# Kernel tuning notes

Measured on AMD Instinct MI355X. Metric: run time of the kernel, lower is better.

## Reference

```python
import jax, jax.numpy as jnp
import numpy as np
import math

D_MODEL = 512
N_HEADS = 8
D_K = D_MODEL // N_HEADS
N_SAMPLES = 16
BETA = 1.0
SCALE = 1.0 / math.sqrt(D_K)
PROPOSAL_TEMP = 0.5


def setup_inputs() -> dict:
    key = jax.random.key(0)
    ks = jax.random.split(key, 9)
    B, S = 2, 512
    x = jax.random.normal(ks[0], (B, S, D_MODEL), dtype=jnp.float32)
    init = lambda k: jax.random.normal(k, (D_MODEL, D_MODEL), dtype=jnp.float32) * 0.02
    return {
        "x": x,
        "Wq": init(ks[1]), "bq": jnp.zeros((D_MODEL,), jnp.float32),
        "Wk": init(ks[2]), "bk": jnp.zeros((D_MODEL,), jnp.float32),
        "Wv": init(ks[3]), "bv": jnp.zeros((D_MODEL,), jnp.float32),
        "Wo": init(ks[4]), "bo": jnp.zeros((D_MODEL,), jnp.float32),
    }


def _importance_sampled_weights(scores):
    # scores: [B,H,S,S]. Replicates the per-row Python loop, fully vectorized.
    B, H, Sq, Sk = scores.shape
    target = jax.nn.softmax(scores * BETA, axis=-1)            # [B,H,Sq,Sk]
    # optimal proposal: 0.5*target + 0.5*uniform
    prop = PROPOSAL_TEMP * target + (1.0 - PROPOSAL_TEMP) / Sk
    R = B * H * Sq
    tf = target.reshape(R, Sk)
    pf = prop.reshape(R, Sk)
    # tsu_backend.sample_binary_layer(log(p/(1-p))) == Bernoulli(p) sampling
    s = jax.random.bernoulli(jax.random.key(42), pf[:, None, :], (R, N_SAMPLES, Sk))
    # importance weight = prod(target[sel]) / (prod(prop[sel]) * prod(1-prop[~sel]))
    pt = jnp.prod(jnp.where(s, tf[:, None, :], 1.0), axis=-1)                 # [R,N]
    pp = jnp.prod(jnp.where(s, pf[:, None, :], 1.0 - pf[:, None, :]), axis=-1)
    valid = (s.sum(-1) > 0) & (pp > 0)
    w = jnp.where(valid, pt / jnp.maximum(pp, 1e-38), 0.0)
    ws = w.sum(-1, keepdims=True)
    w = jnp.where(ws > 0, w / jnp.maximum(ws, 1e-38), 1.0 / N_SAMPLES)        # [R,N]
    wa = jnp.einsum('rn,rnk->rk', w, s.astype(jnp.float32))                   # [R,Sk]
    was = wa.sum(-1, keepdims=True)
    wa = jnp.where(was > 0, wa / jnp.maximum(was, 1e-38), 1.0 / Sk)
    return wa.reshape(B, H, Sq, Sk)


def reference(x, Wq, bq, Wk, bk, Wv, bv, Wo, bo):
    B, S, Dm = x.shape
    proj = lambda W, b: (x @ W + b).reshape(B, S, N_HEADS, D_K).transpose(0, 2, 1, 3)
    Q = proj(Wq, bq)  # [B,H,S,dk]
    K = proj(Wk, bk)
    V = proj(Wv, bv)
    scores = jnp.einsum('bhqd,bhkd->bhqk', Q, K) * SCALE
    # torch builds weights via torch.tensor(...) which detaches => constant w.r.t. params
    attn = jax.lax.stop_gradient(_importance_sampled_weights(scores))
    out = jnp.einsum('bhqk,bhkd->bhqd', attn, V)
    out = out.transpose(0, 2, 1, 3).reshape(B, S, Dm)
    return out @ Wo + bo
```

## Files before the change

### kernel.cpp

```cpp
#include <hip/hip_runtime.h>
#include <cstdint>
#include <cstddef>


#define ROTL(x, r) __builtin_rotateleft32((x), (r))

#define QR8(s)                                                                \
  x0[0]+=x1[0];x0[1]+=x1[1];x0[2]+=x1[2];x0[3]+=x1[3];                        \
  x0[4]+=x1[4];x0[5]+=x1[5];x0[6]+=x1[6];x0[7]+=x1[7];                        \
  x1[0]=ROTL(x1[0],s);x1[1]=ROTL(x1[1],s);x1[2]=ROTL(x1[2],s);                \
  x1[3]=ROTL(x1[3],s);x1[4]=ROTL(x1[4],s);x1[5]=ROTL(x1[5],s);                \
  x1[6]=ROTL(x1[6],s);x1[7]=ROTL(x1[7],s);                                    \
  x1[0]^=x0[0];x1[1]^=x0[1];x1[2]^=x0[2];x1[3]^=x0[3];                        \
  x1[4]^=x0[4];x1[5]^=x0[5];x1[6]^=x0[6];x1[7]^=x0[7];
#define INJ8(X, Y)                                                            \
  x0[0]+=(X);x0[1]+=(X);x0[2]+=(X);x0[3]+=(X);                                \
  x0[4]+=(X);x0[5]+=(X);x0[6]+=(X);x0[7]+=(X);                                \
  x1[0]+=(Y);x1[1]+=(Y);x1[2]+=(Y);x1[3]+=(Y);                                \
  x1[4]+=(Y);x1[5]+=(Y);x1[6]+=(Y);x1[7]+=(Y);
#define INJ8Y(Y)                                                              \
  x1[0]+=(Y);x1[1]+=(Y);x1[2]+=(Y);x1[3]+=(Y);                                \
  x1[4]+=(Y);x1[5]+=(Y);x1[6]+=(Y);x1[7]+=(Y);

__global__ __launch_bounds__(256)
void qkv_gemm(const float* __restrict__ x,
              const float* __restrict__ Wq, const float* __restrict__ bq,
              const float* __restrict__ Wk, const float* __restrict__ bk,
              const float* __restrict__ Wv, const float* __restrict__ bv,
              const float* __restrict__ bo, float* __restrict__ outp,
              float* __restrict__ Qw, float* __restrict__ KTw,
              float* __restrict__ Vw) {
  const int tid = threadIdx.x;
  if (blockIdx.z == 3) {
    const int blk = blockIdx.y * 16 + blockIdx.x;
    const size_t base4 = (size_t)blk * 1024 + tid;
    const float4* bo4 = (const float4*)bo;
    float4* out4 = (float4*)outp;
#pragma unroll
    for (int i = 0; i < 4; ++i) {
      const size_t idx4 = base4 + (size_t)i * 256;
      out4[idx4] = bo4[idx4 & 127];
    }
    return;
  }
  const float* W; const float* bias;
  if (blockIdx.z == 0)      { W = Wq; bias = bq; }
  else if (blockIdx.z == 1) { W = Wk; bias = bk; }
  else                      { W = Wv; bias = bv; }

  __shared__ __align__(16) float smem[64 * 68];
  float (*At)[68] = (float(*)[68])smem;
  float (*Bs)[64] = (float(*)[64])(smem + 32 * 68);
  float (*T2)[68] = (float(*)[68])smem;

  const int tx = tid & 15, ty = tid >> 4;
  const int row0 = blockIdx.x * 64, col0 = blockIdx.y * 64;
  float acc[4][4] = {};

  for (int kk = 0; kk < 512; kk += 32) {
    const int ar = tid >> 2;
#pragma unroll
    for (int i = 0; i < 2; ++i) {
      const int kc = ((tid & 3) << 3) + (i << 2);
      const float4 a4 =
          *(const float4*)&x[(size_t)(row0 + ar) * 512 + kk + kc];
      At[kc + 0][ar] = a4.x; At[kc + 1][ar] = a4.y;
      At[kc + 2][ar] = a4.z; At[kc + 3][ar] = a4.w;
    }
#pragma unroll
    for (int i = 0; i < 2; ++i) {
      const int idx = tid + (i << 8);
      const int br = idx >> 4, bc = (idx & 15) << 2;
      *(float4*)&Bs[br][bc] =
          *(const float4*)&W[(size_t)(kk + br) * 512 + col0 + bc];
    }
    __syncthreads();
#pragma unroll
    for (int p = 0; p < 32; ++p) {
      const float4 a4 = *(const float4*)&At[p][ty << 2];
      const float4 b4 = *(const float4*)&Bs[p][tx << 2];
      acc[0][0] = fmaf(a4.x, b4.x, acc[0][0]); acc[0][1] = fmaf(a4.x, b4.y, acc[0][1]);
      acc[0][2] = fmaf(a4.x, b4.z, acc[0][2]); acc[0][3] = fmaf(a4.x, b4.w, acc[0][3]);
      acc[1][0] = fmaf(a4.y, b4.x, acc[1][0]); acc[1][1] = fmaf(a4.y, b4.y, acc[1][1]);
      acc[1][2] = fmaf(a4.y, b4.z, acc[1][2]); acc[1][3] = fmaf(a4.y, b4.w, acc[1][3]);
      acc[2][0] = fmaf(a4.z, b4.x, acc[2][0]); acc[2][1] = fmaf(a4.z, b4.y, acc[2][1]);
      acc[2][2] = fmaf(a4.z, b4.z, acc[2][2]); acc[2][3] = fmaf(a4.z, b4.w, acc[2][3]);
      acc[3][0] = fmaf(a4.w, b4.x, acc[3][0]); acc[3][1] = fmaf(a4.w, b4.y, acc[3][1]);
      acc[3][2] = fmaf(a4.w, b4.z, acc[3][2]); acc[3][3] = fmaf(a4.w, b4.w, acc[3][3]);
    }
    __syncthreads();
  }

  if (blockIdx.z == 0) {
#pragma unroll
    for (int i = 0; i < 4; ++i) {
      const int row = row0 + (ty << 2) + i;
      const int b = row >> 9, s = row & 511;
#pragma unroll
      for (int j = 0; j < 4; ++j) {
        const int col = col0 + (tx << 2) + j;
        const int h = col >> 6, d = col & 63;
        Qw[(((size_t)(b * 8 + h) * 512 + s) * 64) + d] = acc[i][j] + bias[col];
      }
    }
  } else if (blockIdx.z == 1) {
#pragma unroll
    for (int i = 0; i < 4; ++i) {
#pragma unroll
      for (int j = 0; j < 4; ++j) {
        const int col = col0 + (tx << 2) + j;
        T2[(tx << 2) + j][(ty << 2) + i] = acc[i][j] + bias[col];
      }
    }
    __syncthreads();
    const int c = tid >> 2, seg = tid & 3;
    const int b = row0 >> 9, h = blockIdx.y;
    const int s0 = (row0 & 511) + (seg << 4);
    float* dst = KTw + (((size_t)(b * 8 + h) * 64 + c) << 9) + s0;
#pragma unroll
    for (int i2 = 0; i2 < 4; ++i2) {
      *(float4*)&dst[i2 << 2] = *(const float4*)&T2[c][(seg << 4) + (i2 << 2)];
    }
  } else {
#pragma unroll
    for (int i = 0; i < 4; ++i) {
      const int row = row0 + (ty << 2) + i;
      const int b = row >> 9, s = row & 511;
#pragma unroll
      for (int j = 0; j < 4; ++j) {
        const int col = col0 + (tx << 2) + j;
        const int h = col >> 6, d = col & 63;
        Vw[(((size_t)(b * 8 + h) * 512 + s) * 64) + d] = acc[i][j] + bias[col];
      }
    }
  }
}

__global__ __launch_bounds__(256)
void fused_sample(const float* __restrict__ Q, const float* __restrict__ KT,
                  const float* __restrict__ V, const float* __restrict__ Wo,
                  float* __restrict__ outp) {
  const int r = ((blockIdx.x & 7) << 10) + (blockIdx.x >> 3);
  const int bh = r >> 9, q = r & 511;
  const int b = r >> 12, h = (r >> 9) & 7;
  const int tid = threadIdx.x;
  __shared__ __align__(16) float qs[64];
  __shared__ float red[8];
  __shared__ float tf[512];
  __shared__ __align__(16) uint32_t pscu2[512];
  __shared__ float wa[512];
  __shared__ float wr[16];
  __shared__ float redc[8];
  __shared__ float psum[4][64];
  __shared__ float o_s[64];
  __shared__ int   list[512];
  __shared__ int   cnt;

  if (tid == 0) cnt = 0;
  if (tid < 64) qs[tid] = Q[((size_t)bh * 512 + q) * 64 + tid];
  __syncthreads();

  float sc[2];
#pragma unroll
  for (int ii = 0; ii < 2; ++ii) {
    const int k = tid + (ii << 8);
    const float* Kp = KT + (size_t)bh * 64 * 512 + k;
    float s = 0.f;
#pragma unroll
    for (int d4 = 0; d4 < 16; ++d4) {
      const float4 qv = ((const float4*)qs)[d4];
      const float k0 = Kp[(size_t)(d4 * 4 + 0) * 512];
      const float k1 = Kp[(size_t)(d4 * 4 + 1) * 512];
      const float k2 = Kp[(size_t)(d4 * 4 + 2) * 512];
      const float k3 = Kp[(size_t)(d4 * 4 + 3) * 512];
      s = fmaf(qv.x, k0, s); s = fmaf(qv.y, k1, s);
      s = fmaf(qv.z, k2, s); s = fmaf(qv.w, k3, s);
    }
    sc[ii] = s * 0.125f;
  }
  float mx = fmaxf(sc[0], sc[1]);
  for (int m = 1; m < 64; m <<= 1) mx = fmaxf(mx, __shfl_xor(mx, m));
  if ((tid & 63) == 0) red[tid >> 6] = mx;
  __syncthreads();
  const float rowmax = fmaxf(fmaxf(red[0], red[1]), fmaxf(red[2], red[3]));
  const float e0 = expf(sc[0] - rowmax);
  const float e1 = expf(sc[1] - rowmax);
  float ssum = e0 + e1;
  for (int m = 1; m < 64; m <<= 1) ssum += __shfl_xor(ssum, m);
  if ((tid & 63) == 0) red[4 + (tid >> 6)] = ssum;
  __syncthreads();
  const float tot = red[4] + red[5] + red[6] + red[7];
  const float t0 = e0 / tot, t1 = e1 / tot;
  tf[tid] = t0; tf[tid + 256] = t1;
  wa[tid] = 0.f; wa[tid + 256] = 0.f;
  {
    const float p0 = fmaf(0.5f, t0, 0.0009765625f);
    const float p1 = fmaf(0.5f, t1, 0.0009765625f);
    {
      const int k = tid;
      pscu2[(((k & 31) >> 2) << 6) + ((k >> 5) << 2) + (k & 3)] =
          ((uint32_t)ceilf(p0 * 8388608.0f)) << 9;
    }
    {
      const int k = tid + 256;
      pscu2[(((k & 31) >> 2) << 6) + ((k >> 5) << 2) + (k & 3)] =
          ((uint32_t)ceilf(p1 * 8388608.0f)) << 9;
    }
    float ql = (1.f - p0) * (1.f - p1);
    for (int m = 1; m < 64; m <<= 1) ql *= __shfl_xor(ql, m);
    if ((tid & 63) == 0) redc[4 + (tid >> 6)] = ql;
  }
  __syncthreads();
  const float Qrow = redc[4] * redc[5] * redc[6] * redc[7];

  const int n = tid >> 4, t = tid & 15;
  const int k0i = t << 5;
  const uint32_t cbase =
      (uint32_t)r * 8192u + (uint32_t)n * 512u + (uint32_t)k0i + 42u;
  uint32_t bits = 0u;
#pragma unroll
  for (int jb = 0; jb < 32; jb += 8) {
    uint32_t x0[8], x1[8];
#pragma unroll
    for (int i = 0; i < 8; ++i) {
      const uint32_t c = cbase + (uint32_t)(jb + i);
      x0[i] = c;
      x1[i] = ROTL(c, 13) ^ c;
    }
    QR8(15) QR8(26) QR8(6)
    INJ8(42u, 0x1BD11BF1u)
    QR8(17) QR8(29) QR8(16) QR8(24)
    INJ8(0x1BD11BF0u, 2u)
    QR8(13) QR8(15) QR8(26) QR8(6)
    INJ8Y(45u)
    QR8(17) QR8(29) QR8(16) QR8(24)
    INJ8(42u, 0x1BD11BF4u)
    QR8(13) QR8(15) QR8(26) QR8(6)
    INJ8(0x1BD11BF0u, 5u)
    const uint4 pA = *(const uint4*)&pscu2[((jb >> 2) << 6) + (t << 2)];
    const uint4 pB = *(const uint4*)&pscu2[(((jb >> 2) + 1) << 6) + (t << 2)];
    bits |= (uint32_t)((x0[0] ^ x1[0]) < pA.x) << (jb + 0);
    bits |= (uint32_t)((x0[1] ^ x1[1]) < pA.y) << (jb + 1);
    bits |= (uint32_t)((x0[2] ^ x1[2]) < pA.z) << (jb + 2);
    bits |= (uint32_t)((x0[3] ^ x1[3]) < pA.w) << (jb + 3);
    bits |= (uint32_t)((x0[4] ^ x1[4]) < pB.x) << (jb + 4);
    bits |= (uint32_t)((x0[5] ^ x1[5]) < pB.y) << (jb + 5);
    bits |= (uint32_t)((x0[6] ^ x1[6]) < pB.z) << (jb + 6);
    bits |= (uint32_t)((x0[7] ^ x1[7]) < pB.w) << (jb + 7);
  }

  float ptl = 1.f, ratl = 1.f;
  int cl = __popc(bits);
  {
    uint32_t bb = bits;
    while (bb) {
      const int j = __builtin_ctz(bb);
      bb &= bb - 1u;
      const float tv = tf[k0i + j];
      const float p = fmaf(0.5f, tv, 0.0009765625f);
      ptl *= tv;
      ratl *= p / (1.f - p);
    }
  }
#pragma unroll
  for (int m = 1; m < 16; m <<= 1) {
    ptl *= __shfl_xor(ptl, m);
    ratl *= __shfl_xor(ratl, m);
    cl += __shfl_xor(cl, m);
  }
  if (t == 0) {
    const float pp = Qrow * ratl;
    wr[n] = (cl > 0 && pp > 0.f) ? (ptl / fmaxf(pp, 1e-38f)) : 0.f;
  }
  __syncthreads();
  float wsum = 0.f;
#pragma unroll
  for (int m2 = 0; m2 < 16; ++m2) wsum += wr[m2];
  const float wn = (wsum > 0.f) ? (wr[n] / fmaxf(wsum, 1e-38f)) : 0.0625f;
  {
    uint32_t bb = bits;
    while (bb) {
      const int j = __builtin_ctz(bb);
      bb &= bb - 1u;
      atomicAdd(&wa[k0i + j], wn);
    }
  }
  __syncthreads();

  float sp = wa[tid] + wa[tid + 256];
  for (int m = 1; m < 64; m <<= 1) sp += __shfl_xor(sp, m);
  if ((tid & 63) == 0) redc[tid >> 6] = sp;
  if (wa[tid] > 0.f)       { const int i = atomicAdd(&cnt, 1); list[i] = tid; }
  if (wa[tid + 256] > 0.f) { const int i = atomicAdd(&cnt, 1); list[i] = tid + 256; }
  __syncthreads();
  const float was = redc[0] + redc[1] + redc[2] + redc[3];
  const int nnz = cnt;

  const int g = tid >> 6, d = tid & 63;
  const float* Vb = V + ((size_t)(b * 8 + h) * 512) * 64;
  float acc = 0.f;
  if (was > 0.f) {
    const float inv = 1.f / fmaxf(was, 1e-38f);
    for (int i = g; i < nnz; i += 4) {
      const int k = list[i];
      acc = fmaf(wa[k] * inv, Vb[(size_t)k * 64 + d], acc);
    }
  } else {
    for (int k = g; k < 512; k += 4) acc += Vb[(size_t)k * 64 + d];
    acc *= 0.001953125f;
  }
  psum[g][d] = acc;
  __syncthreads();
  if (g == 0)
    o_s[d] = psum[0][d] + psum[1][d] + psum[2][d] + psum[3][d];
  __syncthreads();

  {
    const float* Wh = Wo + ((size_t)h * 64) * 512;
    float a0 = 0.f, a1 = 0.f;
#pragma unroll 8
    for (int dd = 0; dd < 64; ++dd) {
      const float ov = o_s[dd];
      a0 = fmaf(ov, Wh[(size_t)dd * 512 + tid], a0);
      a1 = fmaf(ov, Wh[(size_t)dd * 512 + tid + 256], a1);
    }
    float* orow = outp + ((size_t)(b * 512 + q)) * 512;
    atomicAdd(&orow[tid], a0);
    atomicAdd(&orow[tid + 256], a1);
  }
}

extern "C" void kernel_launch(void* const* d_in, const int* in_sizes, int n_in,
                              void* d_out, int out_size, void* d_ws,
                              size_t ws_size, hipStream_t stream) {
  const float* x  = (const float*)d_in[0];
  const float* Wq = (const float*)d_in[1];
  const float* bq = (const float*)d_in[2];
  const float* Wk = (const float*)d_in[3];
  const float* bk = (const float*)d_in[4];
  const float* Wv = (const float*)d_in[5];
  const float* bv = (const float*)d_in[6];
  const float* Wo = (const float*)d_in[7];
  const float* bo = (const float*)d_in[8];
  float* out = (float*)d_out;

  float* ws = (float*)d_ws;
  float* Qw = ws;
  float* KT = ws + 524288;
  float* Vw = ws + 1048576;

  dim3 gq(16, 8, 4);
  qkv_gemm<<<gq, 256, 0, stream>>>(x, Wq, bq, Wk, bk, Wv, bv, bo, out,
                                   Qw, KT, Vw);
  fused_sample<<<8192, 256, 0, stream>>>(Qw, KT, Vw, Wo, out);
}
```

Measured before the change: 253.0 us.

## Map one attention row per wavefront and register-prefetch smaller QKV GEMM tiles

The sampling kernel now handles four query rows per block, one per 64-lane wavefront, so block-wide __syncthreads and shared reductions become shuffles and wave-local LDS fences. Each lane computes eight scores with float4 K loads, builds 128 sample bits across two 64-bit masks, and does the Wo projection with eight accumulators using shuffled o values. The QKV GEMM uses 32-row tiles with register prefetch of the next k-slice to double the grid and overlap loads. The cost is more per-lane serial work (longer Philox loops and ctz loops) and reliance on wave-synchronous LDS semantics.

```diff
diff --git a/kernel.cpp b/kernel.cpp
--- a/kernel.cpp
+++ b/kernel.cpp
@@ -22,6 +22,8 @@
   x1[0]+=(Y);x1[1]+=(Y);x1[2]+=(Y);x1[3]+=(Y);                                \
   x1[4]+=(Y);x1[5]+=(Y);x1[6]+=(Y);x1[7]+=(Y);
 
+#define WAVE_FENCE() asm volatile("s_waitcnt lgkmcnt(0)" ::: "memory")
+
 __global__ __launch_bounds__(256)
 void qkv_gemm(const float* __restrict__ x,
               const float* __restrict__ Wq, const float* __restrict__ bq,
@@ -32,15 +34,12 @@
               float* __restrict__ Vw) {
   const int tid = threadIdx.x;
   if (blockIdx.z == 3) {
-    const int blk = blockIdx.y * 16 + blockIdx.x;
-    const size_t base4 = (size_t)blk * 1024 + tid;
+    const int blk = blockIdx.y * 32 + blockIdx.x;
+    const size_t base4 = (size_t)blk * 512 + tid;
     const float4* bo4 = (const float4*)bo;
     float4* out4 = (float4*)outp;
-#pragma unroll
-    for (int i = 0; i < 4; ++i) {
-      const size_t idx4 = base4 + (size_t)i * 256;
-      out4[idx4] = bo4[idx4 & 127];
-    }
+    out4[base4] = bo4[base4 & 127];
+    out4[base4 + 256] = bo4[(base4 + 256) & 127];
     return;
   }
   const float* W; const float* bias;
@@ -48,90 +47,81 @@
   else if (blockIdx.z == 1) { W = Wk; bias = bk; }
   else                      { W = Wv; bias = bv; }
 
-  __shared__ __align__(16) float smem[64 * 68];
-  float (*At)[68] = (float(*)[68])smem;
-  float (*Bs)[64] = (float(*)[64])(smem + 32 * 68);
-  float (*T2)[68] = (float(*)[68])smem;
+  __shared__ __align__(16) float smem[32 * 34 + 32 * 64];
+  float (*At)[34] = (float(*)[34])smem;
+  float (*Bs)[64] = (float(*)[64])(smem + 32 * 34);
+  float (*T2)[34] = (float(*)[34])smem;
 
   const int tx = tid & 15, ty = tid >> 4;
-  const int row0 = blockIdx.x * 64, col0 = blockIdx.y * 64;
-  float acc[4][4] = {};
+  const int row0 = blockIdx.x * 32, col0 = blockIdx.y * 64;
+  float acc[2][4] = {};
+
+  const int ar = tid >> 3;
+  const int kc = (tid & 7) << 2;
+  const int br0 = tid >> 4,         bc0 = (tid & 15) << 2;
+  const int br1 = (tid + 256) >> 4, bc1 = ((tid + 256) & 15) << 2;
+
+  float4 aR, bR0, bR1;
+  aR  = *(const float4*)&x[(size_t)(row0 + ar) * 512 + kc];
+  bR0 = *(const float4*)&W[(size_t)br0 * 512 + col0 + bc0];
+  bR1 = *(const float4*)&W[(size_t)br1 * 512 + col0 + bc1];
 
   for (int kk = 0; kk < 512; kk += 32) {
-    const int ar = tid >> 2;
+    At[kc + 0][ar] = aR.x; At[kc + 1][ar] = aR.y;
+    At[kc + 2][ar] = aR.z; At[kc + 3][ar] = aR.w;
+    *(float4*)&Bs[br0][bc0] = bR0;
+    *(float4*)&Bs[br1][bc1] = bR1;
+    __syncthreads();
+    if (kk < 480) {
+      const int kn = kk + 32;
+      aR  = *(const float4*)&x[(size_t)(row0 + ar) * 512 + kn + kc];
+      bR0 = *(const float4*)&W[(size_t)(kn + br0) * 512 + col0 + bc0];
+      bR1 = *(const float4*)&W[(size_t)(kn + br1) * 512 + col0 + bc1];
+    }
+#pragma unroll
+    for (int p = 0; p < 32; ++p) {
+      const float2 a2 = *(const float2*)&At[p][ty << 1];
+      const float4 b4 = *(const float4*)&Bs[p][tx << 2];
+      acc[0][0] = fmaf(a2.x, b4.x, acc[0][0]); acc[0][1] = fmaf(a2.x, b4.y, acc[0][1]);
+      acc[0][2] = fmaf(a2.x, b4.z, acc[0][2]); acc[0][3] = fmaf(a2.x, b4.w, acc[0][3]);
+      acc[1][0] = fmaf(a2.y, b4.x, acc[1][0]); acc[1][1] = fmaf(a2.y, b4.y, acc[1][1]);
+      acc[1][2] = fmaf(a2.y, b4.z, acc[1][2]); acc[1][3] = fmaf(a2.y, b4.w, acc[1][3]);
+    }
+    __syncthreads();
+  }
+
+  const int h = blockIdx.y;
+  if (blockIdx.z == 0 || blockIdx.z == 2) {
+    float* dst = (blockIdx.z == 0) ? Qw : Vw;
 #pragma unroll
     for (int i = 0; i < 2; ++i) {
-      const int kc = ((tid & 3) << 3) + (i << 2);
-      const float4 a4 =
-          *(const float4*)&x[(size_t)(row0 + ar) * 512 + kk + kc];
-      At[kc + 0][ar] = a4.x; At[kc + 1][ar] = a4.y;
-      At[kc + 2][ar] = a4.z; At[kc + 3][ar] = a4.w;
-    }
-#pragma unroll
-    for (int i = 0; i < 2; ++i) {
-      const int idx = tid + (i << 8);
-      const int br = idx >> 4, bc = (idx & 15) << 2;
-      *(float4*)&Bs[br][bc] =
-          *(const float4*)&W[(size_t)(kk + br) * 512 + col0 + bc];
-    }
-    __syncthreads();
-#pragma unroll
-    for (int p = 0; p < 32; ++p) {
-      const float4 a4 = *(const float4*)&At[p][ty << 2];
-      const float4 b4 = *(const float4*)&Bs[p][tx << 2];
-      acc[0][0] = fmaf(a4.x, b4.x, acc[0][0]); acc[0][1] = fmaf(a4.x, b4.y, acc[0][1]);
-      acc[0][2] = fmaf(a4.x, b4.z, acc[0][2]); acc[0][3] = fmaf(a4.x, b4.w, acc[0][3]);
-      acc[1][0] = fmaf(a4.y, b4.x, acc[1][0]); acc[1][1] = fmaf(a4.y, b4.y, acc[1][1]);
-      acc[1][2] = fmaf(a4.y, b4.z, acc[1][2]); acc[1][3] = fmaf(a4.y, b4.w, acc[1][3]);
-      acc[2][0] = fmaf(a4.z, b4.x, acc[2][0]); acc[2][1] = fmaf(a4.z, b4.y, acc[2][1]);
-      acc[2][2] = fmaf(a4.z, b4.z, acc[2][2]); acc[2][3] = fmaf(a4.z, b4.w, acc[2][3]);
-      acc[3][0] = fmaf(a4.w, b4.x, acc[3][0]); acc[3][1] = fmaf(a4.w, b4.y, acc[3][1]);
-      acc[3][2] = fmaf(a4.w, b4.z, acc[3][2]); acc[3][3] = fmaf(a4.w, b4.w, acc[3][3]);
-    }
-    __syncthreads();
-  }
-
-  if (blockIdx.z == 0) {
-#pragma unroll
-    for (int i = 0; i < 4; ++i) {
-      const int row = row0 + (ty << 2) + i;
+      const int row = row0 + (ty << 1) + i;
       const int b = row >> 9, s = row & 511;
 #pragma unroll
       for (int j = 0; j < 4; ++j) {
         const int col = col0 + (tx << 2) + j;
-        const int h = col >> 6, d = col & 63;
-        Qw[(((size_t)(b * 8 + h) * 512 + s) * 64) + d] = acc[i][j] + bias[col];
+        const int d = col & 63;
+        dst[(((size_t)(b * 8 + h) * 512 + s) * 64) + d] = acc[i][j] + bias[col];
       }
     }
-  } else if (blockIdx.z == 1) {
-#pragma unroll
-    for (int i = 0; i < 4; ++i) {
+  } else {
+#pragma unroll
+    for (int i = 0; i < 2; ++i) {
 #pragma unroll
       for (int j = 0; j < 4; ++j) {
         const int col = col0 + (tx << 2) + j;
-        T2[(tx << 2) + j][(ty << 2) + i] = acc[i][j] + bias[col];
+        T2[(tx << 2) + j][(ty << 1) + i] = acc[i][j] + bias[col];
       }
     }
     __syncthreads();
-    const int c = tid >> 2, seg = tid & 3;
-    const int b = row0 >> 9, h = blockIdx.y;
-    const int s0 = (row0 & 511) + (seg << 4);
-    float* dst = KTw + (((size_t)(b * 8 + h) * 64 + c) << 9) + s0;
-#pragma unroll
-    for (int i2 = 0; i2 < 4; ++i2) {
-      *(float4*)&dst[i2 << 2] = *(const float4*)&T2[c][(seg << 4) + (i2 << 2)];
-    }
-  } else {
-#pragma unroll
-    for (int i = 0; i < 4; ++i) {
-      const int row = row0 + (ty << 2) + i;
-      const int b = row >> 9, s = row & 511;
-#pragma unroll
-      for (int j = 0; j < 4; ++j) {
-        const int col = col0 + (tx << 2) + j;
-        const int h = col >> 6, d = col & 63;
-        Vw[(((size_t)(b * 8 + h) * 512 + s) * 64) + d] = acc[i][j] + bias[col];
-      }
+    const int b = row0 >> 9;
+    const int s0 = row0 & 511;
+#pragma unroll
+    for (int i2 = 0; i2 < 2; ++i2) {
+      const int idx = tid + (i2 << 8);
+      const int c = idx >> 3, seg = idx & 7;
+      float* dst = KTw + (((size_t)(b * 8 + h) * 64 + c) << 9) + s0 + (seg << 2);
+      *(float4*)dst = *(const float4*)&T2[c][seg << 2];
     }
   }
 }
@@ -140,90 +130,102 @@
 void fused_sample(const float* __restrict__ Q, const float* __restrict__ KT,
                   const float* __restrict__ V, const float* __restrict__ Wo,
                   float* __restrict__ outp) {
-  const int r = ((blockIdx.x & 7) << 10) + (blockIdx.x >> 3);
+  const int tid = threadIdx.x;
+  const int w = tid >> 6, l = tid & 63;
+  const int blk = blockIdx.x;
+  const int swz = ((blk & 7) << 8) | (blk >> 3);
+  const int r = (swz << 2) + w;
   const int bh = r >> 9, q = r & 511;
   const int b = r >> 12, h = (r >> 9) & 7;
-  const int tid = threadIdx.x;
-  __shared__ __align__(16) float qs[64];
-  __shared__ float red[8];
-  __shared__ float tf[512];
-  __shared__ __align__(16) uint32_t pscu2[512];
-  __shared__ float wa[512];
-  __shared__ float wr[16];
-  __shared__ float redc[8];
-  __shared__ float psum[4][64];
-  __shared__ float o_s[64];
-  __shared__ int   list[512];
-  __shared__ int   cnt;
-
-  if (tid == 0) cnt = 0;
-  if (tid < 64) qs[tid] = Q[((size_t)bh * 512 + q) * 64 + tid];
-  __syncthreads();
-
-  float sc[2];
-#pragma unroll
-  for (int ii = 0; ii < 2; ++ii) {
-    const int k = tid + (ii << 8);
-    const float* Kp = KT + (size_t)bh * 64 * 512 + k;
-    float s = 0.f;
-#pragma unroll
+
+  __shared__ __align__(16) float    qs[4][64];
+  __shared__ __align__(16) float    tfs[4][512];
+  __shared__ __align__(16) uint32_t thru[4][512];
+
+  float* tf = tfs[w];
+  uint32_t* thr = thru[w];
+  uint4* thr4 = (uint4*)thr;
+  float* wa = (float*)thr;
+
+  qs[w][l] = Q[((size_t)bh * 512 + q) * 64 + l];
+  WAVE_FENCE();
+
+  float s0 = 0.f, s1 = 0.f, s2 = 0.f, s3 = 0.f;
+  float s4 = 0.f, s5 = 0.f, s6 = 0.f, s7 = 0.f;
+  {
+    const float* Kp = KT + (size_t)bh * 64 * 512 + (l << 2);
+#pragma unroll 4
     for (int d4 = 0; d4 < 16; ++d4) {
-      const float4 qv = ((const float4*)qs)[d4];
-      const float k0 = Kp[(size_t)(d4 * 4 + 0) * 512];
-      const float k1 = Kp[(size_t)(d4 * 4 + 1) * 512];
-      const float k2 = Kp[(size_t)(d4 * 4 + 2) * 512];
-      const float k3 = Kp[(size_t)(d4 * 4 + 3) * 512];
-      s = fmaf(qv.x, k0, s); s = fmaf(qv.y, k1, s);
-      s = fmaf(qv.z, k2, s); s = fmaf(qv.w, k3, s);
-    }
-    sc[ii] = s * 0.125f;
-  }
-  float mx = fmaxf(sc[0], sc[1]);
+      const float4 qv = *(const float4*)&qs[w][d4 << 2];
+#pragma unroll
+      for (int c = 0; c < 4; ++c) {
+        const float qd = (c == 0) ? qv.x : (c == 1) ? qv.y : (c == 2) ? qv.z : qv.w;
+        const size_t off = (size_t)(d4 * 4 + c) * 512;
+        const float4 ka = *(const float4*)&Kp[off];
+        const float4 kb = *(const float4*)&Kp[off + 256];
+        s0 = fmaf(qd, ka.x, s0); s1 = fmaf(qd, ka.y, s1);
+        s2 = fmaf(qd, ka.z, s2); s3 = fmaf(qd, ka.w, s3);
+        s4 = fmaf(qd, kb.x, s4); s5 = fmaf(qd, kb.y, s5);
+        s6 = fmaf(qd, kb.z, s6); s7 = fmaf(qd, kb.w, s7);
+      }
+    }
+    s0 *= 0.125f; s1 *= 0.125f; s2 *= 0.125f; s3 *= 0.125f;
+    s4 *= 0.125f; s5 *= 0.125f; s6 *= 0.125f; s7 *= 0.125f;
+  }
+
+  float mx = fmaxf(fmaxf(fmaxf(s0, s1), fmaxf(s2, s3)),
+                   fmaxf(fmaxf(s4, s5), fmaxf(s6, s7)));
+#pragma unroll
   for (int m = 1; m < 64; m <<= 1) mx = fmaxf(mx, __shfl_xor(mx, m));
-  if ((tid & 63) == 0) red[tid >> 6] = mx;
-  __syncthreads();
-  const float rowmax = fmaxf(fmaxf(red[0], red[1]), fmaxf(red[2], red[3]));
-  const float e0 = expf(sc[0] - rowmax);
-  const float e1 = expf(sc[1] - rowmax);
-  float ssum = e0 + e1;
-  for (int m = 1; m < 64; m <<= 1) ssum += __shfl_xor(ssum, m);
-  if ((tid & 63) == 0) red[4 + (tid >> 6)] = ssum;
-  __syncthreads();
-  const float tot = red[4] + red[5] + red[6] + red[7];
-  const float t0 = e0 / tot, t1 = e1 / tot;
-  tf[tid] = t0; tf[tid + 256] = t1;
-  wa[tid] = 0.f; wa[tid + 256] = 0.f;
-  {
-    const float p0 = fmaf(0.5f, t0, 0.0009765625f);
-    const float p1 = fmaf(0.5f, t1, 0.0009765625f);
-    {
-      const int k = tid;
-      pscu2[(((k & 31) >> 2) << 6) + ((k >> 5) << 2) + (k & 3)] =
-          ((uint32_t)ceilf(p0 * 8388608.0f)) << 9;
-    }
-    {
-      const int k = tid + 256;
-      pscu2[(((k & 31) >> 2) << 6) + ((k >> 5) << 2) + (k & 3)] =
-          ((uint32_t)ceilf(p1 * 8388608.0f)) << 9;
-    }
-    float ql = (1.f - p0) * (1.f - p1);
-    for (int m = 1; m < 64; m <<= 1) ql *= __shfl_xor(ql, m);
-    if ((tid & 63) == 0) redc[4 + (tid >> 6)] = ql;
-  }
-  __syncthreads();
-  const float Qrow = redc[4] * redc[5] * redc[6] * redc[7];
-
-  const int n = tid >> 4, t = tid & 15;
-  const int k0i = t << 5;
+  const float e0 = expf(s0 - mx), e1 = expf(s1 - mx);
+  const float e2 = expf(s2 - mx), e3 = expf(s3 - mx);
+  const float e4 = expf(s4 - mx), e5 = expf(s5 - mx);
+  const float e6 = expf(s6 - mx), e7 = expf(s7 - mx);
+  float tot = ((e0 + e1) + (e2 + e3)) + ((e4 + e5) + (e6 + e7));
+#pragma unroll
+  for (int m = 1; m < 64; m <<= 1) tot += __shfl_xor(tot, m);
+  const float t0 = e0 / tot, t1 = e1 / tot, t2 = e2 / tot, t3 = e3 / tot;
+  const float t4 = e4 / tot, t5 = e5 / tot, t6 = e6 / tot, t7 = e7 / tot;
+  const float p0 = fmaf(0.5f, t0, 0.0009765625f);
+  const float p1 = fmaf(0.5f, t1, 0.0009765625f);
+  const float p2 = fmaf(0.5f, t2, 0.0009765625f);
+  const float p3 = fmaf(0.5f, t3, 0.0009765625f);
+  const float p4 = fmaf(0.5f, t4, 0.0009765625f);
+  const float p5 = fmaf(0.5f, t5, 0.0009765625f);
+  const float p6 = fmaf(0.5f, t6, 0.0009765625f);
+  const float p7 = fmaf(0.5f, t7, 0.0009765625f);
+  {
+    *(float4*)&tf[l << 2]         = make_float4(t0, t1, t2, t3);
+    *(float4*)&tf[256 + (l << 2)] = make_float4(t4, t5, t6, t7);
+    uint4 ta, tb;
+    ta.x = ((uint32_t)ceilf(p0 * 8388608.0f)) << 9;
+    ta.y = ((uint32_t)ceilf(p1 * 8388608.0f)) << 9;
+    ta.z = ((uint32_t)ceilf(p2 * 8388608.0f)) << 9;
+    ta.w = ((uint32_t)ceilf(p3 * 8388608.0f)) << 9;
+    tb.x = ((uint32_t)ceilf(p4 * 8388608.0f)) << 9;
+    tb.y = ((uint32_t)ceilf(p5 * 8388608.0f)) << 9;
+    tb.z = ((uint32_t)ceilf(p6 * 8388608.0f)) << 9;
+    tb.w = ((uint32_t)ceilf(p7 * 8388608.0f)) << 9;
+    thr4[((l & 31) << 2) + (l >> 5)]     = ta;
+    thr4[((l & 31) << 2) + (l >> 5) + 2] = tb;
+  }
+  float ql = (((1.f - p0) * (1.f - p1)) * ((1.f - p2) * (1.f - p3))) *
+             (((1.f - p4) * (1.f - p5)) * ((1.f - p6) * (1.f - p7)));
+#pragma unroll
+  for (int m = 1; m < 64; m <<= 1) ql *= __shfl_xor(ql, m);
+  const float Qrow = ql;
+  WAVE_FENCE();
+
+  const int n = l >> 2, gl = l & 3;
   const uint32_t cbase =
-      (uint32_t)r * 8192u + (uint32_t)n * 512u + (uint32_t)k0i + 42u;
-  uint32_t bits = 0u;
-#pragma unroll
-  for (int jb = 0; jb < 32; jb += 8) {
+      (uint32_t)r * 8192u + (uint32_t)n * 512u + (uint32_t)(gl << 7) + 42u;
+  unsigned long long lo = 0ull, hi = 0ull;
+  for (int u = 0; u < 16; ++u) {
     uint32_t x0[8], x1[8];
+    const uint32_t cb = cbase + (uint32_t)(u << 3);
 #pragma unroll
     for (int i = 0; i < 8; ++i) {
-      const uint32_t c = cbase + (uint32_t)(jb + i);
+      const uint32_t c = cb + (uint32_t)i;
       x0[i] = c;
       x1[i] = ROTL(c, 13) ^ c;
     }
@@ -237,96 +239,131 @@
     INJ8(42u, 0x1BD11BF4u)
     QR8(13) QR8(15) QR8(26) QR8(6)
     INJ8(0x1BD11BF0u, 5u)
-    const uint4 pA = *(const uint4*)&pscu2[((jb >> 2) << 6) + (t << 2)];
-    const uint4 pB = *(const uint4*)&pscu2[(((jb >> 2) + 1) << 6) + (t << 2)];
-    bits |= (uint32_t)((x0[0] ^ x1[0]) < pA.x) << (jb + 0);
-    bits |= (uint32_t)((x0[1] ^ x1[1]) < pA.y) << (jb + 1);
-    bits |= (uint32_t)((x0[2] ^ x1[2]) < pA.z) << (jb + 2);
-    bits |= (uint32_t)((x0[3] ^ x1[3]) < pA.w) << (jb + 3);
-    bits |= (uint32_t)((x0[4] ^ x1[4]) < pB.x) << (jb + 4);
-    bits |= (uint32_t)((x0[5] ^ x1[5]) < pB.y) << (jb + 5);
-    bits |= (uint32_t)((x0[6] ^ x1[6]) < pB.z) << (jb + 6);
-    bits |= (uint32_t)((x0[7] ^ x1[7]) < pB.w) << (jb + 7);
+    const uint4 pA = thr4[(u << 3) + gl];
+    const uint4 pB = thr4[(u << 3) + 4 + gl];
+    uint32_t byte = 0u;
+    byte |= (uint32_t)((x0[0] ^ x1[0]) < pA.x) << 0;
+    byte |= (uint32_t)((x0[1] ^ x1[1]) < pA.y) << 1;
+    byte |= (uint32_t)((x0[2] ^ x1[2]) < pA.z) << 2;
+    byte |= (uint32_t)((x0[3] ^ x1[3]) < pA.w) << 3;
+    byte |= (uint32_t)((x0[4] ^ x1[4]) < pB.x) << 4;
+    byte |= (uint32_t)((x0[5] ^ x1[5]) < pB.y) << 5;
+    byte |= (uint32_t)((x0[6] ^ x1[6]) < pB.z) << 6;
+    byte |= (uint32_t)((x0[7] ^ x1[7]) < pB.w) << 7;
+    const int sh = (u & 7) << 3;
+    if (u < 8) lo |= (unsigned long long)byte << sh;
+    else       hi |= (unsigned long long)byte << sh;
   }
 
   float ptl = 1.f, ratl = 1.f;
-  int cl = __popc(bits);
-  {
-    uint32_t bb = bits;
+  int cl = __popcll(lo) + __popcll(hi);
+  {
+    unsigned long long bb = lo;
     while (bb) {
-      const int j = __builtin_ctz(bb);
-      bb &= bb - 1u;
-      const float tv = tf[k0i + j];
+      const int j = __builtin_ctzll(bb);
+      bb &= bb - 1ull;
+      const float tv = tf[(gl << 7) + j];
       const float p = fmaf(0.5f, tv, 0.0009765625f);
       ptl *= tv;
       ratl *= p / (1.f - p);
     }
-  }
-#pragma unroll
-  for (int m = 1; m < 16; m <<= 1) {
+    bb = hi;
+    while (bb) {
+      const int j = __builtin_ctzll(bb);
+      bb &= bb - 1ull;
+      const float tv = tf[(gl << 7) + 64 + j];
+      const float p = fmaf(0.5f, tv, 0.0009765625f);
+      ptl *= tv;
+      ratl *= p / (1.f - p);
+    }
+  }
+#pragma unroll
+  for (int m = 1; m < 4; m <<= 1) {
     ptl *= __shfl_xor(ptl, m);
     ratl *= __shfl_xor(ratl, m);
     cl += __shfl_xor(cl, m);
   }
-  if (t == 0) {
-    const float pp = Qrow * ratl;
-    wr[n] = (cl > 0 && pp > 0.f) ? (ptl / fmaxf(pp, 1e-38f)) : 0.f;
-  }
-  __syncthreads();
-  float wsum = 0.f;
-#pragma unroll
-  for (int m2 = 0; m2 < 16; ++m2) wsum += wr[m2];
-  const float wn = (wsum > 0.f) ? (wr[n] / fmaxf(wsum, 1e-38f)) : 0.0625f;
-  {
-    uint32_t bb = bits;
+  const float pp = Qrow * ratl;
+  const float wl = (cl > 0 && pp > 0.f) ? (ptl / fmaxf(pp, 1e-38f)) : 0.f;
+  float wsum = (gl == 0) ? wl : 0.f;
+#pragma unroll
+  for (int m = 1; m < 64; m <<= 1) wsum += __shfl_xor(wsum, m);
+  const float wn = (wsum > 0.f) ? (wl / fmaxf(wsum, 1e-38f)) : 0.0625f;
+
+  WAVE_FENCE();
+  *(float4*)&wa[l << 2]         = make_float4(0.f, 0.f, 0.f, 0.f);
+  *(float4*)&wa[256 + (l << 2)] = make_float4(0.f, 0.f, 0.f, 0.f);
+  WAVE_FENCE();
+  {
+    unsigned long long bb = lo;
     while (bb) {
-      const int j = __builtin_ctz(bb);
-      bb &= bb - 1u;
-      atomicAdd(&wa[k0i + j], wn);
-    }
-  }
-  __syncthreads();
-
-  float sp = wa[tid] + wa[tid + 256];
+      const int j = __builtin_ctzll(bb);
+      bb &= bb - 1ull;
+      atomicAdd(&wa[(gl << 7) + j], wn);
+    }
+    bb = hi;
+    while (bb) {
+      const int j = __builtin_ctzll(bb);
+      bb &= bb - 1ull;
+      atomicAdd(&wa[(gl << 7) + 64 + j], wn);
+    }
+  }
+  WAVE_FENCE();
+
+  float sp = 0.f;
+#pragma unroll
+  for (int c = 0; c < 8; ++c) sp += wa[(c << 6) + l];
+#pragma unroll
   for (int m = 1; m < 64; m <<= 1) sp += __shfl_xor(sp, m);
-  if ((tid & 63) == 0) redc[tid >> 6] = sp;
-  if (wa[tid] > 0.f)       { const int i = atomicAdd(&cnt, 1); list[i] = tid; }
-  if (wa[tid + 256] > 0.f) { const int i = atomicAdd(&cnt, 1); list[i] = tid + 256; }
-  __syncthreads();
-  const float was = redc[0] + redc[1] + redc[2] + redc[3];
-  const int nnz = cnt;
-
-  const int g = tid >> 6, d = tid & 63;
+  const float was = sp;
+
   const float* Vb = V + ((size_t)(b * 8 + h) * 512) * 64;
-  float acc = 0.f;
+  float o = 0.f;
   if (was > 0.f) {
     const float inv = 1.f / fmaxf(was, 1e-38f);
-    for (int i = g; i < nnz; i += 4) {
-      const int k = list[i];
-      acc = fmaf(wa[k] * inv, Vb[(size_t)k * 64 + d], acc);
+#pragma unroll 1
+    for (int c = 0; c < 8; ++c) {
+      const float v = wa[(c << 6) + l];
+      unsigned long long mask = __ballot(v > 0.f);
+      while (mask) {
+        const int j = __builtin_ctzll(mask);
+        mask &= mask - 1ull;
+        const int k = (c << 6) + j;
+        const float wv = wa[k];
+        o = fmaf(wv * inv, Vb[(size_t)k * 64 + l], o);
+      }
     }
   } else {
-    for (int k = g; k < 512; k += 4) acc += Vb[(size_t)k * 64 + d];
-    acc *= 0.001953125f;
-  }
-  psum[g][d] = acc;
-  __syncthreads();
-  if (g == 0)
-    o_s[d] = psum[0][d] + psum[1][d] + psum[2][d] + psum[3][d];
-  __syncthreads();
-
-  {
-    const float* Wh = Wo + ((size_t)h * 64) * 512;
-    float a0 = 0.f, a1 = 0.f;
-#pragma unroll 8
+    for (int k = 0; k < 512; ++k) o += Vb[(size_t)k * 64 + l];
+    o *= 0.001953125f;
+  }
+
+  {
+    const float* Wh = Wo + ((size_t)h * 64) * 512 + l;
+    float a0 = 0.f, a1 = 0.f, a2 = 0.f, a3 = 0.f;
+    float a4 = 0.f, a5 = 0.f, a6 = 0.f, a7 = 0.f;
+#pragma unroll 4
     for (int dd = 0; dd < 64; ++dd) {
-      const float ov = o_s[dd];
-      a0 = fmaf(ov, Wh[(size_t)dd * 512 + tid], a0);
-      a1 = fmaf(ov, Wh[(size_t)dd * 512 + tid + 256], a1);
-    }
-    float* orow = outp + ((size_t)(b * 512 + q)) * 512;
-    atomicAdd(&orow[tid], a0);
-    atomicAdd(&orow[tid + 256], a1);
+      const float ov = __shfl(o, dd);
+      const float* wrow = Wh + (size_t)dd * 512;
+      a0 = fmaf(ov, wrow[0],   a0);
+      a1 = fmaf(ov, wrow[64],  a1);
+      a2 = fmaf(ov, wrow[128], a2);
+      a3 = fmaf(ov, wrow[192], a3);
+      a4 = fmaf(ov, wrow[256], a4);
+      a5 = fmaf(ov, wrow[320], a5);
+      a6 = fmaf(ov, wrow[384], a6);
+      a7 = fmaf(ov, wrow[448], a7);
+    }
+    float* orow = outp + ((size_t)(b * 512 + q)) * 512 + l;
+    atomicAdd(&orow[0],   a0);
+    atomicAdd(&orow[64],  a1);
+    atomicAdd(&orow[128], a2);
+    atomicAdd(&orow[192], a3);
+    atomicAdd(&orow[256], a4);
+    atomicAdd(&orow[320], a5);
+    atomicAdd(&orow[384], a6);
+    atomicAdd(&orow[448], a7);
   }
 }
 
@@ -349,8 +386,8 @@
   float* KT = ws + 524288;
   float* Vw = ws + 1048576;
 
-  dim3 gq(16, 8, 4);
+  dim3 gq(32, 8, 4);
   qkv_gemm<<<gq, 256, 0, stream>>>(x, Wq, bq, Wk, bk, Wv, bv, bo, out,
                                    Qw, KT, Vw);
-  fused_sample<<<8192, 256, 0, stream>>>(Qw, KT, Vw, Wo, out);
+  fused_sample<<<2048, 256, 0, stream>>>(Qw, KT, Vw, Wo, out);
 }
```

Result: slower. 283.4 us (+12.0%).
